# Kernel optimization log

Hardware: AMD Instinct MI355X
Metric: run time of the kernel (lower is better)

Reference implementation:

```python
import jax, jax.numpy as jnp
import numpy as np

B, T, IN, H, K = 128, 4096, 2, 64, 2  # batch, seq_len, input feat, lstm hidden, num tags


def setup_inputs() -> dict:
    key = jax.random.key(0)
    ks = jax.random.split(key, 16)
    s = 1.0 / np.sqrt(H)
    u = lambda k, shape, a: jax.random.uniform(k, shape, jnp.float32, -a, a)
    p = {}
    p['x'] = jax.random.normal(ks[0], (B, T, IN), jnp.float32)
    # layer 0 (input IN), layer 1 (input 2H); leading dim 2 = [forward, backward] direction
    p['w_ih0'] = u(ks[1], (2, 4 * H, IN), s)
    p['w_hh0'] = u(ks[2], (2, 4 * H, H), s)
    p['b_ih0'] = u(ks[3], (2, 4 * H), s)
    p['b_hh0'] = u(ks[4], (2, 4 * H), s)
    p['w_ih1'] = u(ks[5], (2, 4 * H, 2 * H), s)
    p['w_hh1'] = u(ks[6], (2, 4 * H, H), s)
    p['b_ih1'] = u(ks[7], (2, 4 * H), s)
    p['b_hh1'] = u(ks[8], (2, 4 * H), s)
    p['fc_w'] = u(ks[9], (K, 2 * H), 1.0 / np.sqrt(2 * H))
    p['fc_b'] = u(ks[10], (K,), 1.0 / np.sqrt(2 * H))
    # CRF params (torchcrf init: U(-0.1, 0.1))
    p['trans'] = u(ks[11], (K, K), 0.1)
    p['start'] = u(ks[12], (K,), 0.1)
    p['end'] = u(ks[13], (K,), 0.1)
    return p


def _lstm_dir(xg, w_hh, b_hh):
    # xg: [T, B, 4H] precomputed input projections; PyTorch gate order i, f, g, o
    b, h = xg.shape[1], w_hh.shape[1]

    def step(carry, g_x):
        hs, cs = carry
        g = g_x + hs @ w_hh.T + b_hh
        i, f, gg, o = jnp.split(g, 4, axis=-1)
        cs = jax.nn.sigmoid(f) * cs + jax.nn.sigmoid(i) * jnp.tanh(gg)
        hs = jax.nn.sigmoid(o) * jnp.tanh(cs)
        return (hs, cs), hs

    init = (jnp.zeros((b, h), xg.dtype), jnp.zeros((b, h), xg.dtype))
    _, out = jax.lax.scan(step, init, xg)
    return out  # [T, B, H]


def _bilstm_layer(xt, w_ih, w_hh, b_ih, b_hh):
    # xt: [T, B, F] time-major input
    xg_f = jnp.einsum('tbi,gi->tbg', xt, w_ih[0]) + b_ih[0]
    xg_b = jnp.einsum('tbi,gi->tbg', xt[::-1], w_ih[1]) + b_ih[1]
    hf = _lstm_dir(xg_f, w_hh[0], b_hh[0])
    hb = _lstm_dir(xg_b, w_hh[1], b_hh[1])[::-1]
    return jnp.concatenate([hf, hb], axis=-1)  # [T, B, 2H]


def _viterbi(logits, trans, start, end):
    # logits: [B, T, K] -> best path [B, T]
    e = jnp.swapaxes(logits, 0, 1)  # [T, B, K]
    score0 = start[None, :] + e[0]

    def fwd(score, e_t):
        cand = score[:, :, None] + trans[None, :, :]  # [B, Kprev, Knext]
        bp = jnp.argmax(cand, axis=1)
        return jnp.max(cand, axis=1) + e_t, bp

    score, bps = jax.lax.scan(fwd, score0, e[1:])  # bps: [T-1, B, K]
    last = jnp.argmax(score + end[None, :], axis=-1)  # [B]

    def back(tag, bp):
        prev = jnp.take_along_axis(bp, tag[:, None], axis=1)[:, 0]
        return prev, prev

    _, path = jax.lax.scan(back, last, bps, reverse=True)  # [T-1, B]
    return jnp.swapaxes(jnp.concatenate([path, last[None, :]], axis=0), 0, 1)


def reference(x, w_ih0, w_hh0, b_ih0, b_hh0, w_ih1, w_hh1, b_ih1, b_hh1,
              fc_w, fc_b, trans, start, end):
    xt = jnp.swapaxes(x, 0, 1)  # [T, B, IN]
    h0 = _bilstm_layer(xt, w_ih0, w_hh0, b_ih0, b_hh0)
    h1 = _bilstm_layer(h0, w_ih1, w_hh1, b_ih1, b_hh1)  # [T, B, 2H]
    logits = jnp.swapaxes(jnp.einsum('tbh,kh->tbk', h1, fc_w) + fc_b, 0, 1)  # [B, T, K]
    return _viterbi(logits, trans, start, end).astype(jnp.int32)
```

## Files before the change

kernel.cpp:

```cpp
#include <hip/hip_runtime.h>

#define TT 4096
#define BATCH 128
#define HID 64
#define CK 32
#define NCH (TT / CK)
#define NSLOT (NCH + 1)
#define TG 64

__device__ __forceinline__ float sigm(float x) { return 1.f / (1.f + expf(-x)); }
__device__ __forceinline__ float tanh_f(float x) { float e = expf(2.f * x); return 1.f - 2.f / (e + 1.f); }

__global__ __launch_bounds__(512, 2) void lstm_ckpt(
    const float* __restrict__ x,
    const float* __restrict__ w_ih,
    const float* __restrict__ w_hh,
    const float* __restrict__ b_ih, const float* __restrict__ b_hh,
    float* __restrict__ ckpt)
{
    const int blk = blockIdx.x;
    const int dir = blk & 1;
    const int b   = blk >> 1;
    const int tid = threadIdx.x;
    const int row = tid >> 1, half = tid & 1;

    __shared__ __align__(16) float xs[TT * 2];
    __shared__ __align__(16) float h_lds[HID];
    __shared__ __align__(16) float g_lds[256];

    {
        const float4* src = (const float4*)(x + (size_t)b * TT * 2);
        float4* dst = (float4*)xs;
        for (int rr = tid; rr < 2048; rr += 512) dst[rr] = src[rr];
    }
    const int grow = dir * 256 + row;
    float wv[32];
    {
        const float4* wr = (const float4*)(w_hh + (size_t)grow * 64) + half * 8;
        #pragma unroll
        for (int k = 0; k < 8; ++k) {
            float4 v = wr[k];
            wv[4*k] = v.x; wv[4*k+1] = v.y; wv[4*k+2] = v.z; wv[4*k+3] = v.w;
        }
    }
    const float wx0 = half ? 0.f : w_ih[grow * 2 + 0];
    const float wx1 = half ? 0.f : w_ih[grow * 2 + 1];
    const float bias = half ? 0.f : (b_ih[grow] + b_hh[grow]);
    const int gtype = row >> 6;
    float c = 0.f, hreg = 0.f;
    if (tid < HID) h_lds[tid] = 0.f;
    __syncthreads();

    for (int t = 0; t < TT; ++t) {
        const int tt = dir ? (TT - 1 - t) : t;
        if (tid < HID) {
            const int bnum = dir ? (tt + 1) : tt;
            if ((bnum & (CK - 1)) == 0) {
                float* cp = ckpt + (((size_t)(dir * BATCH + b) * NSLOT + (bnum >> 5)) << 7);
                cp[tid] = hreg; cp[HID + tid] = c;
            }
        }
        const float4* h4 = (const float4*)h_lds + half * 8;
        float a0 = 0.f, a1 = 0.f, a2 = 0.f, a3 = 0.f;
        #pragma unroll
        for (int k = 0; k < 8; ++k) {
            float4 hv = h4[k];
            a0 = fmaf(wv[4*k],   hv.x, a0);
            a1 = fmaf(wv[4*k+1], hv.y, a1);
            a2 = fmaf(wv[4*k+2], hv.z, a2);
            a3 = fmaf(wv[4*k+3], hv.w, a3);
        }
        float tot = (a0 + a1) + (a2 + a3);
        tot += __shfl_xor(tot, 1);
        if (half == 0) {
            const float acc = tot + bias + wx0 * xs[tt * 2] + wx1 * xs[tt * 2 + 1];
            g_lds[row] = (gtype == 2) ? tanh_f(acc) : sigm(acc);
        }
        __syncthreads();
        if (tid < HID) {
            const float iv = g_lds[tid], fv = g_lds[64 + tid], gg = g_lds[128 + tid], ov = g_lds[192 + tid];
            c = fv * c + iv * gg;
            hreg = ov * tanh_f(c);
            h_lds[tid] = hreg;
        }
        __syncthreads();
    }
}

__global__ __launch_bounds__(256, 4) void l0_xg(
    const float* __restrict__ x,
    const float* __restrict__ w_ih0, const float* __restrict__ w_hh0,
    const float* __restrict__ b_ih0, const float* __restrict__ b_hh0,
    const float* __restrict__ w_ih1, const float* __restrict__ b_ih1,
    const float* __restrict__ ckpt,
    float* __restrict__ xg,
    int slab_t0)
{
    const int ntg = gridDim.x / BATCH;
    const int b  = blockIdx.x / ntg;
    const int tg = blockIdx.x % ntg;
    const int T0 = slab_t0 + tg * TG;
    const int tid = threadIdx.x;
    const int e = tid & 63;
    const int cupd = tid >> 6;

    __shared__ __align__(16) float h0b[TG][128];
    __shared__ __align__(16) float hs[2][64];
    __shared__ __align__(16) float gg[2][256];
    __shared__ __align__(16) float xb[TG][2];

    if (tid < 32)
        ((float4*)xb)[tid] = ((const float4*)(x + ((size_t)b * TT + T0) * 2))[tid];

    float wl0[64];
    for (int dir = 0; dir < 2; ++dir) {
        const int rowg = dir * 256 + tid;
        {
            const float4* wa = (const float4*)(w_hh0 + (size_t)rowg * 64);
            #pragma unroll
            for (int k = 0; k < 16; ++k) {
                float4 v = wa[k];
                wl0[4*k] = v.x; wl0[4*k+1] = v.y; wl0[4*k+2] = v.z; wl0[4*k+3] = v.w;
            }
        }
        const float wx0 = w_ih0[rowg * 2 + 0], wx1 = w_ih0[rowg * 2 + 1];
        const float biasr = b_ih0[rowg] + b_hh0[rowg];
        float c_st = 0.f;
        if (tid < 128) {
            const int C = T0 / CK + cupd;
            const int slot = dir ? (C + 1) : C;
            const float* cp = ckpt + (((size_t)(dir * BATCH + b) * NSLOT + slot) << 7);
            hs[cupd][e] = cp[e];
            c_st = cp[HID + e];
        }
        __syncthreads();
        for (int s = 0; s < CK; ++s) {
            float res[2];
            #pragma unroll
            for (int c = 0; c < 2; ++c) {
                const float4* h4 = (const float4*)hs[c];
                float a0 = 0.f, a1 = 0.f, a2 = 0.f, a3 = 0.f;
                #pragma unroll
                for (int k = 0; k < 16; ++k) {
                    float4 hv = h4[k];
                    a0 = fmaf(wl0[4*k],   hv.x, a0);
                    a1 = fmaf(wl0[4*k+1], hv.y, a1);
                    a2 = fmaf(wl0[4*k+2], hv.z, a2);
                    a3 = fmaf(wl0[4*k+3], hv.w, a3);
                }
                const int tl = c * CK + (dir ? (CK - 1 - s) : s);
                res[c] = biasr + ((a0 + a1) + (a2 + a3)) + wx0 * xb[tl][0] + wx1 * xb[tl][1];
            }
            #pragma unroll
            for (int c = 0; c < 2; ++c)
                gg[c][tid] = ((tid >> 6) == 2) ? tanh_f(res[c]) : sigm(res[c]);
            __syncthreads();
            if (tid < 128) {
                const float iv = gg[cupd][e], fv = gg[cupd][64 + e], g2 = gg[cupd][128 + e], ov = gg[cupd][192 + e];
                c_st = fv * c_st + iv * g2;
                const float hv = ov * tanh_f(c_st);
                const int tl = cupd * CK + (dir ? (CK - 1 - s) : s);
                hs[cupd][e] = hv;
                h0b[tl][dir * 64 + e] = hv;
            }
            __syncthreads();
        }
    }
    for (int l1dir = 0; l1dir < 2; ++l1dir) {
        const float4* wrow = (const float4*)(w_ih1 + (size_t)(l1dir * 256 + tid) * 128);
        const float br = b_ih1[l1dir * 256 + tid];
        for (int halfT = 0; halfT < 2; ++halfT) {
            float acc[32];
            #pragma unroll
            for (int s2 = 0; s2 < 32; ++s2) acc[s2] = br;
            for (int kq = 0; kq < 32; ++kq) {
                float4 wc = wrow[kq];
                #pragma unroll
                for (int s2 = 0; s2 < 32; ++s2) {
                    float4 hv = *(const float4*)&h0b[halfT * 32 + s2][kq * 4];
                    acc[s2] = fmaf(wc.w, hv.w, fmaf(wc.z, hv.z, fmaf(wc.y, hv.y, fmaf(wc.x, hv.x, acc[s2]))));
                }
            }
            for (int s2 = 0; s2 < 32; ++s2) {
                const int tl = halfT * 32 + s2;
                xg[(((size_t)(tg * TG + tl) * BATCH + b) * 2 + l1dir) * 256 + tid] = acc[s2];
            }
        }
    }
}

__global__ __launch_bounds__(256, 2) void lstm_l1(
    const float* __restrict__ w_hh1, const float* __restrict__ b_hh1,
    const float* __restrict__ fc_w,
    const float* __restrict__ xg,
    float* __restrict__ hc1,
    float* __restrict__ plog,
    int slab_t0, int slabT)
{
    const int blk = blockIdx.x;
    const int l1dir = blk & 1;
    const int b = blk >> 1;
    const int tid = threadIdx.x;
    const int lane = tid & 63;

    __shared__ __align__(16) float h1b[2][HID];
    __shared__ __align__(16) float g1[256];
    __shared__ __align__(16) float xq[4][256];

    float wl1[64];
    {
        const int grow = l1dir * 256 + tid;
        const float4* wh = (const float4*)(w_hh1 + (size_t)grow * 64);
        #pragma unroll
        for (int k = 0; k < 16; ++k) {
            float4 v = wh[k];
            wl1[4*k] = v.x; wl1[4*k+1] = v.y; wl1[4*k+2] = v.z; wl1[4*k+3] = v.w;
        }
    }
    const float bias1 = b_hh1[l1dir * 256 + tid];
    float fw0 = 0.f, fw1 = 0.f;
    if (tid >= 64 && tid < 128) {
        fw0 = fc_w[l1dir * 64 + lane];
        fw1 = fc_w[128 + l1dir * 64 + lane];
    }
    float c1 = 0.f;
    float* hcme = hc1 + (size_t)blk * 128;
    if (tid < 64) {
        if (slab_t0 == 0) { h1b[0][tid] = 0.f; c1 = 0.f; }
        else { h1b[0][tid] = hcme[tid]; c1 = hcme[64 + tid]; }
    }
    const float* xgb = xg + ((size_t)b * 2 + l1dir) * 256;
    const size_t tstride = (size_t)BATCH * 2 * 256;
    if (tid < 128) {
        const int stp = tid >> 6;
        if (stp < slabT)
            ((float4*)xq[stp])[lane] = ((const float4*)(xgb + (size_t)stp * tstride))[lane];
    }
    float4 pend = make_float4(0.f, 0.f, 0.f, 0.f);
    if (tid >= 64 && tid < 192) {
        const int tgt = (tid < 128) ? 2 : 3;
        if (tgt < slabT) pend = ((const float4*)(xgb + (size_t)tgt * tstride))[lane];
    }
    __syncthreads();

    for (int tt = 0; tt < slabT; ++tt) {
        const int u = slab_t0 + tt;
        const int cur = tt & 1;
        {
            const float4* h4 = (const float4*)h1b[cur];
            float a0 = 0.f, a1 = 0.f, a2 = 0.f, a3 = 0.f;
            #pragma unroll
            for (int k = 0; k < 16; ++k) {
                float4 hv = h4[k];
                a0 = fmaf(wl1[4*k],   hv.x, a0);
                a1 = fmaf(wl1[4*k+1], hv.y, a1);
                a2 = fmaf(wl1[4*k+2], hv.z, a2);
                a3 = fmaf(wl1[4*k+3], hv.w, a3);
            }
            const float acc = bias1 + xq[tt & 3][tid] + ((a0 + a1) + (a2 + a3));
            g1[tid] = ((tid >> 6) == 2) ? tanh_f(acc) : sigm(acc);
        }
        __syncthreads();
        if (tid < 64) {
            const float iv = g1[tid], fv = g1[64 + tid], gg = g1[128 + tid], ov = g1[192 + tid];
            c1 = fv * c1 + iv * gg;
            h1b[cur ^ 1][tid] = ov * tanh_f(c1);
        } else if (tid < 192) {
            if (tid < 128 && u > 0) {
                const float hv = h1b[cur][lane];
                float p0 = hv * fw0, p1 = hv * fw1;
                #pragma unroll
                for (int d_ = 32; d_ > 0; d_ >>= 1) { p0 += __shfl_xor(p0, d_); p1 += __shfl_xor(p1, d_); }
                if (lane == 0) {
                    const int tp = l1dir ? (TT - u) : (u - 1);
                    *(float2*)(plog + (((size_t)l1dir * BATCH + b) * TT + tp) * 2) = make_float2(p0, p1);
                }
            }
            const int par = (tid < 128) ? 0 : 1;
            if ((tt & 1) == par) {
                if (tt + 2 < slabT) ((float4*)xq[(tt + 2) & 3])[lane] = pend;
                if (tt + 4 < slabT) pend = ((const float4*)(xgb + (size_t)(tt + 4) * tstride))[lane];
            }
        }
        __syncthreads();
    }
    if (tid < 64) { hcme[tid] = h1b[slabT & 1][tid]; hcme[64 + tid] = c1; }
    if (slab_t0 + slabT == TT && tid >= 64 && tid < 128) {
        const float hv = h1b[slabT & 1][lane];
        float p0 = hv * fw0, p1 = hv * fw1;
        #pragma unroll
        for (int d_ = 32; d_ > 0; d_ >>= 1) { p0 += __shfl_xor(p0, d_); p1 += __shfl_xor(p1, d_); }
        if (lane == 0) {
            const int tp = l1dir ? 0 : (TT - 1);
            *(float2*)(plog + (((size_t)l1dir * BATCH + b) * TT + tp) * 2) = make_float2(p0, p1);
        }
    }
}

__device__ __forceinline__ unsigned long long shfl_u64(unsigned long long v, int src) {
    unsigned int lo = (unsigned int)v, hi = (unsigned int)(v >> 32);
    lo = __shfl(lo, src); hi = __shfl(hi, src);
    return ((unsigned long long)hi << 32) | lo;
}

__global__ __launch_bounds__(64, 1) void viterbi_k(
    const float* __restrict__ plog, const float* __restrict__ fc_b,
    const float* __restrict__ trans, const float* __restrict__ startv,
    const float* __restrict__ endv, int* __restrict__ out)
{
    const int b = blockIdx.x;
    const int lane = threadIdx.x;
    __shared__ __align__(16) float2 e_lds[64][65];

    const float fb0 = fc_b[0], fb1 = fc_b[1];
    const float* pf = plog + ((size_t)(0 * BATCH + b) * TT) * 2;
    const float* pb = plog + ((size_t)(1 * BATCH + b) * TT) * 2;
    for (int r = 0; r < 32; ++r) {
        const int i4 = r * 64 + lane;
        float4 a = ((const float4*)pf)[i4];
        float4 cc = ((const float4*)pb)[i4];
        const int t0 = 2 * i4, t1 = t0 + 1;
        e_lds[t0 & 63][t0 >> 6] = make_float2(a.x + cc.x + fb0, a.y + cc.y + fb1);
        e_lds[t1 & 63][t1 >> 6] = make_float2(a.z + cc.z + fb0, a.w + cc.w + fb1);
    }
    __syncthreads();
    const float tr00 = trans[0], tr01 = trans[1], tr10 = trans[2], tr11 = trans[3];
    const float2 e0 = e_lds[0][0];
    const float s00 = startv[0] + e0.x, s01 = startv[1] + e0.y;

    const int lo = lane * 64;
    const int hi = (lane == 63) ? (TT - 1) : (lo + 64);
    float a00, a01, a10, a11;
    {
        const float2 ee = e_lds[(lo + 1) & 63][(lo + 1) >> 6];
        a00 = tr00 + ee.x; a01 = tr01 + ee.y; a10 = tr10 + ee.x; a11 = tr11 + ee.y;
    }
    for (int t = lo + 2; t <= hi; ++t) {
        const float2 ee = e_lds[t & 63][t >> 6];
        const float n00 = fmaxf(a00 + tr00, a01 + tr10) + ee.x;
        const float n01 = fmaxf(a00 + tr01, a01 + tr11) + ee.y;
        const float n10 = fmaxf(a10 + tr00, a11 + tr10) + ee.x;
        const float n11 = fmaxf(a10 + tr01, a11 + tr11) + ee.y;
        a00 = n00; a01 = n01; a10 = n10; a11 = n11;
    }
    #pragma unroll
    for (int d = 1; d < 64; d <<= 1) {
        const float o00 = __shfl_up(a00, d), o01 = __shfl_up(a01, d);
        const float o10 = __shfl_up(a10, d), o11 = __shfl_up(a11, d);
        if (lane >= d) {
            const float n00 = fmaxf(o00 + a00, o01 + a10);
            const float n01 = fmaxf(o00 + a01, o01 + a11);
            const float n10 = fmaxf(o10 + a00, o11 + a10);
            const float n11 = fmaxf(o10 + a01, o11 + a11);
            a00 = n00; a01 = n01; a10 = n10; a11 = n11;
        }
    }
    const float p00 = __shfl_up(a00, 1), p01 = __shfl_up(a01, 1);
    const float p10 = __shfl_up(a10, 1), p11 = __shfl_up(a11, 1);
    float s0, s1;
    if (lane == 0) { s0 = s00; s1 = s01; }
    else { s0 = fmaxf(s00 + p00, s01 + p10); s1 = fmaxf(s00 + p01, s01 + p11); }
    unsigned long long m0 = 0ull, m1 = 0ull;
    for (int t = lo + 1; t <= hi; ++t) {
        const float2 ee = e_lds[t & 63][t >> 6];
        const float c00 = s0 + tr00, c10 = s1 + tr10;
        const float c01 = s0 + tr01, c11 = s1 + tr11;
        const int bp0 = c10 > c00, bp1 = c11 > c01;
        s0 = (bp0 ? c10 : c00) + ee.x;
        s1 = (bp1 ? c11 : c01) + ee.y;
        m0 |= (unsigned long long)bp0 << (t - lo - 1);
        m1 |= (unsigned long long)bp1 << (t - lo - 1);
    }
    int last;
    {
        const int lt = (s1 + endv[1]) > (s0 + endv[0]);
        last = __shfl(lt, 63);
    }
    int f0 = 0, f1 = 1;
    for (int t = hi; t > lo; --t) {
        const int s_ = t - lo - 1;
        f0 = (int)(((f0 ? m1 : m0) >> s_) & 1ull);
        f1 = (int)(((f1 ? m1 : m0) >> s_) & 1ull);
    }
    int mm = f0 | (f1 << 1);
    #pragma unroll
    for (int d = 1; d < 64; d <<= 1) {
        const int mo = __shfl_down(mm, d);
        if (lane + d < 64) {
            const int r0 = (mm >> (mo & 1)) & 1;
            const int r1_ = (mm >> ((mo >> 1) & 1)) & 1;
            mm = r0 | (r1_ << 1);
        }
    }
    const int gn = __shfl_down(mm, 1);
    int cur = (lane == 63) ? last : ((gn >> last) & 1);
    unsigned long long tagm = 0ull;
    if (lane == 63) tagm |= (unsigned long long)last << 63;
    for (int t = hi; t > lo; --t) {
        const int s_ = t - lo - 1;
        cur = (int)(((cur ? m1 : m0) >> s_) & 1ull);
        tagm |= (unsigned long long)cur << s_;
    }
    int* ob = out + (size_t)b * TT;
    for (int r = 0; r < 64; ++r) {
        const unsigned long long mr = shfl_u64(tagm, r);
        ob[r * 64 + lane] = (int)((mr >> lane) & 1ull);
    }
}

extern "C" void kernel_launch(void* const* d_in, const int* in_sizes, int n_in,
                              void* d_out, int out_size, void* d_ws, size_t ws_size,
                              hipStream_t stream) {
    const float* x      = (const float*)d_in[0];
    const float* w_ih0  = (const float*)d_in[1];
    const float* w_hh0  = (const float*)d_in[2];
    const float* b_ih0  = (const float*)d_in[3];
    const float* b_hh0  = (const float*)d_in[4];
    const float* w_ih1  = (const float*)d_in[5];
    const float* w_hh1  = (const float*)d_in[6];
    const float* b_ih1  = (const float*)d_in[7];
    const float* b_hh1  = (const float*)d_in[8];
    const float* fc_w   = (const float*)d_in[9];
    const float* fc_b   = (const float*)d_in[10];
    const float* trans  = (const float*)d_in[11];
    const float* startv = (const float*)d_in[12];
    const float* endv   = (const float*)d_in[13];

    char* ws = (char*)d_ws;
    const size_t ckpt_bytes = (size_t)2 * BATCH * NSLOT * 128 * 4;
    const size_t plog_bytes = (size_t)2 * BATCH * TT * 2 * 4;
    const size_t hc1_bytes  = (size_t)256 * 128 * 4;
    float* ckpt = (float*)ws;
    float* plog = (float*)(ws + ckpt_bytes);
    float* hc1  = (float*)(ws + ckpt_bytes + plog_bytes);
    float* xg   = (float*)(ws + ckpt_bytes + plog_bytes + hc1_bytes);

    const size_t perT = (size_t)BATCH * 2 * 256 * 4;
    const size_t fixed = ckpt_bytes + plog_bytes + hc1_bytes;
    size_t avail = (ws_size > fixed) ? (ws_size - fixed) : 0;
    int slabT = (int)(avail / perT);
    slabT = (slabT / TG) * TG;
    if (slabT > TT) slabT = TT;
    if (slabT < TG) slabT = TG;

    lstm_ckpt<<<256, 512, 0, stream>>>(x, w_ih0, w_hh0, b_ih0, b_hh0, ckpt);
    for (int t0 = 0; t0 < TT; t0 += slabT) {
        const int curT = (TT - t0 < slabT) ? (TT - t0) : slabT;
        l0_xg<<<BATCH * (curT / TG), 256, 0, stream>>>(x, w_ih0, w_hh0, b_ih0, b_hh0,
                                                       w_ih1, b_ih1, ckpt, xg, t0);
        lstm_l1<<<256, 256, 0, stream>>>(w_hh1, b_hh1, fc_w, xg, hc1, plog, t0, curT);
    }
    viterbi_k<<<128, 64, 0, stream>>>(plog, fc_b, trans, startv, endv, (int*)d_out);
}
```

Before: 8.860 ms.

## Exchange LSTM gates via warp shuffles to drop one barrier per timestep

Both recurrent LSTM kernels now place each hidden unit's four gate rows in the same group of 8 adjacent lanes. The gates are combined with xor shuffles instead of going through shared memory, which removes one __syncthreads per timestep and double-buffers h. Layer 1 grows from 256 to 576 threads: 512 threads split each gate dot product in half, and a separate 64-thread wave handles the FC projection and the xg prefetch. In exchange, every thread now runs the cell-update transcendentals redundantly, and the larger block may limit occupancy.

```diff
diff --git a/kernel.cpp b/kernel.cpp
--- a/kernel.cpp
+++ b/kernel.cpp
@@ -22,67 +22,71 @@
     const int dir = blk & 1;
     const int b   = blk >> 1;
     const int tid = threadIdx.x;
-    const int row = tid >> 1, half = tid & 1;
+    const int e    = tid >> 3;
+    const int q    = (tid >> 1) & 3;
+    const int half = tid & 1;
+    const int sub  = tid & 7;
 
     __shared__ __align__(16) float xs[TT * 2];
-    __shared__ __align__(16) float h_lds[HID];
-    __shared__ __align__(16) float g_lds[256];
+    __shared__ __align__(16) float hb[2][HID];
 
     {
         const float4* src = (const float4*)(x + (size_t)b * TT * 2);
         float4* dst = (float4*)xs;
         for (int rr = tid; rr < 2048; rr += 512) dst[rr] = src[rr];
     }
-    const int grow = dir * 256 + row;
-    float wv[32];
+    const int row = dir * 256 + q * 64 + e;
+    float wl[32];
     {
-        const float4* wr = (const float4*)(w_hh + (size_t)grow * 64) + half * 8;
+        const float4* wr = (const float4*)(w_hh + (size_t)row * 64) + half * 8;
         #pragma unroll
         for (int k = 0; k < 8; ++k) {
             float4 v = wr[k];
-            wv[4*k] = v.x; wv[4*k+1] = v.y; wv[4*k+2] = v.z; wv[4*k+3] = v.w;
-        }
-    }
-    const float wx0 = half ? 0.f : w_ih[grow * 2 + 0];
-    const float wx1 = half ? 0.f : w_ih[grow * 2 + 1];
-    const float bias = half ? 0.f : (b_ih[grow] + b_hh[grow]);
-    const int gtype = row >> 6;
-    float c = 0.f, hreg = 0.f;
-    if (tid < HID) h_lds[tid] = 0.f;
+            wl[4*k] = v.x; wl[4*k+1] = v.y; wl[4*k+2] = v.z; wl[4*k+3] = v.w;
+        }
+    }
+    const float wx0 = w_ih[row * 2 + 0], wx1 = w_ih[row * 2 + 1];
+    const float bias = b_ih[row] + b_hh[row];
+    float c = 0.f, h = 0.f;
+    if (tid < HID) hb[0][tid] = 0.f;
     __syncthreads();
 
     for (int t = 0; t < TT; ++t) {
         const int tt = dir ? (TT - 1 - t) : t;
-        if (tid < HID) {
+        const int cur = t & 1;
+        {
             const int bnum = dir ? (tt + 1) : tt;
-            if ((bnum & (CK - 1)) == 0) {
+            if ((bnum & (CK - 1)) == 0 && sub == 0) {
                 float* cp = ckpt + (((size_t)(dir * BATCH + b) * NSLOT + (bnum >> 5)) << 7);
-                cp[tid] = hreg; cp[HID + tid] = c;
-            }
-        }
-        const float4* h4 = (const float4*)h_lds + half * 8;
+                cp[e] = h; cp[HID + e] = c;
+            }
+        }
+        const float4* h4 = (const float4*)hb[cur] + half * 8;
         float a0 = 0.f, a1 = 0.f, a2 = 0.f, a3 = 0.f;
         #pragma unroll
         for (int k = 0; k < 8; ++k) {
             float4 hv = h4[k];
-            a0 = fmaf(wv[4*k],   hv.x, a0);
-            a1 = fmaf(wv[4*k+1], hv.y, a1);
-            a2 = fmaf(wv[4*k+2], hv.z, a2);
-            a3 = fmaf(wv[4*k+3], hv.w, a3);
+            a0 = fmaf(wl[4*k],   hv.x, a0);
+            a1 = fmaf(wl[4*k+1], hv.y, a1);
+            a2 = fmaf(wl[4*k+2], hv.z, a2);
+            a3 = fmaf(wl[4*k+3], hv.w, a3);
         }
         float tot = (a0 + a1) + (a2 + a3);
         tot += __shfl_xor(tot, 1);
-        if (half == 0) {
-            const float acc = tot + bias + wx0 * xs[tt * 2] + wx1 * xs[tt * 2 + 1];
-            g_lds[row] = (gtype == 2) ? tanh_f(acc) : sigm(acc);
-        }
-        __syncthreads();
-        if (tid < HID) {
-            const float iv = g_lds[tid], fv = g_lds[64 + tid], gg = g_lds[128 + tid], ov = g_lds[192 + tid];
-            c = fv * c + iv * gg;
-            hreg = ov * tanh_f(c);
-            h_lds[tid] = hreg;
-        }
+        const float2 xv = *(const float2*)&xs[tt * 2];
+        tot += bias + wx0 * xv.x + wx1 * xv.y;
+        const float av = (q == 2) ? tanh_f(tot) : sigm(tot);
+        const float bv = __shfl_xor(av, 2);
+        const float cv = __shfl_xor(av, 4);
+        const float dv = __shfl_xor(bv, 4);
+        float iv, fv, gv, ov;
+        if      (q == 0) { iv = av; fv = bv; gv = cv; ov = dv; }
+        else if (q == 1) { iv = bv; fv = av; gv = dv; ov = cv; }
+        else if (q == 2) { iv = cv; fv = dv; gv = av; ov = bv; }
+        else             { iv = dv; fv = cv; gv = bv; ov = av; }
+        c = fv * c + iv * gv;
+        h = ov * tanh_f(c);
+        if (sub == 0) hb[cur ^ 1][e] = h;
         __syncthreads();
     }
 }
@@ -189,7 +193,7 @@
     }
 }
 
-__global__ __launch_bounds__(256, 2) void lstm_l1(
+__global__ __launch_bounds__(576, 1) void lstm_l1(
     const float* __restrict__ w_hh1, const float* __restrict__ b_hh1,
     const float* __restrict__ fc_w,
     const float* __restrict__ xg,
@@ -201,96 +205,104 @@
     const int l1dir = blk & 1;
     const int b = blk >> 1;
     const int tid = threadIdx.x;
-    const int lane = tid & 63;
+    const bool isGate = tid < 512;
+    const int e    = tid >> 3;
+    const int q    = (tid >> 1) & 3;
+    const int half = tid & 1;
+    const int sub  = tid & 7;
+    const int lane9 = tid - 512;
 
     __shared__ __align__(16) float h1b[2][HID];
-    __shared__ __align__(16) float g1[256];
     __shared__ __align__(16) float xq[4][256];
 
-    float wl1[64];
-    {
-        const int grow = l1dir * 256 + tid;
-        const float4* wh = (const float4*)(w_hh1 + (size_t)grow * 64);
-        #pragma unroll
-        for (int k = 0; k < 16; ++k) {
-            float4 v = wh[k];
-            wl1[4*k] = v.x; wl1[4*k+1] = v.y; wl1[4*k+2] = v.z; wl1[4*k+3] = v.w;
-        }
-    }
-    const float bias1 = b_hh1[l1dir * 256 + tid];
-    float fw0 = 0.f, fw1 = 0.f;
-    if (tid >= 64 && tid < 128) {
-        fw0 = fc_w[l1dir * 64 + lane];
-        fw1 = fc_w[128 + l1dir * 64 + lane];
-    }
-    float c1 = 0.f;
-    float* hcme = hc1 + (size_t)blk * 128;
-    if (tid < 64) {
-        if (slab_t0 == 0) { h1b[0][tid] = 0.f; c1 = 0.f; }
-        else { h1b[0][tid] = hcme[tid]; c1 = hcme[64 + tid]; }
-    }
+    float wl[32];
+    float bias1 = 0.f, fw0 = 0.f, fw1 = 0.f;
+    float c1 = 0.f, h = 0.f;
+    float4 pend0 = make_float4(0.f,0.f,0.f,0.f), pend1 = make_float4(0.f,0.f,0.f,0.f);
     const float* xgb = xg + ((size_t)b * 2 + l1dir) * 256;
     const size_t tstride = (size_t)BATCH * 2 * 256;
-    if (tid < 128) {
-        const int stp = tid >> 6;
-        if (stp < slabT)
-            ((float4*)xq[stp])[lane] = ((const float4*)(xgb + (size_t)stp * tstride))[lane];
-    }
-    float4 pend = make_float4(0.f, 0.f, 0.f, 0.f);
-    if (tid >= 64 && tid < 192) {
-        const int tgt = (tid < 128) ? 2 : 3;
-        if (tgt < slabT) pend = ((const float4*)(xgb + (size_t)tgt * tstride))[lane];
+    float* hcme = hc1 + (size_t)blk * 128;
+
+    if (isGate) {
+        const int grow = l1dir * 256 + q * 64 + e;
+        const float4* wr = (const float4*)(w_hh1 + (size_t)grow * 64) + half * 8;
+        #pragma unroll
+        for (int k = 0; k < 8; ++k) {
+            float4 v = wr[k];
+            wl[4*k] = v.x; wl[4*k+1] = v.y; wl[4*k+2] = v.z; wl[4*k+3] = v.w;
+        }
+        bias1 = b_hh1[grow];
+        if (slab_t0 == 0) { h = 0.f; c1 = 0.f; }
+        else { h = hcme[e]; c1 = hcme[64 + e]; }
+        if (sub == 0) h1b[0][e] = h;
+    } else {
+        fw0 = fc_w[l1dir * 64 + lane9];
+        fw1 = fc_w[128 + l1dir * 64 + lane9];
+        #pragma unroll
+        for (int s = 0; s < 3; ++s)
+            if (s < slabT)
+                ((float4*)xq[s])[lane9] = ((const float4*)(xgb + (size_t)s * tstride))[lane9];
+        if (3 < slabT) pend0 = ((const float4*)(xgb + (size_t)3 * tstride))[lane9];
+        if (4 < slabT) pend1 = ((const float4*)(xgb + (size_t)4 * tstride))[lane9];
     }
     __syncthreads();
 
     for (int tt = 0; tt < slabT; ++tt) {
-        const int u = slab_t0 + tt;
         const int cur = tt & 1;
-        {
-            const float4* h4 = (const float4*)h1b[cur];
+        if (isGate) {
+            const float4* h4 = (const float4*)h1b[cur] + half * 8;
             float a0 = 0.f, a1 = 0.f, a2 = 0.f, a3 = 0.f;
             #pragma unroll
-            for (int k = 0; k < 16; ++k) {
+            for (int k = 0; k < 8; ++k) {
                 float4 hv = h4[k];
-                a0 = fmaf(wl1[4*k],   hv.x, a0);
-                a1 = fmaf(wl1[4*k+1], hv.y, a1);
-                a2 = fmaf(wl1[4*k+2], hv.z, a2);
-                a3 = fmaf(wl1[4*k+3], hv.w, a3);
-            }
-            const float acc = bias1 + xq[tt & 3][tid] + ((a0 + a1) + (a2 + a3));
-            g1[tid] = ((tid >> 6) == 2) ? tanh_f(acc) : sigm(acc);
-        }
-        __syncthreads();
-        if (tid < 64) {
-            const float iv = g1[tid], fv = g1[64 + tid], gg = g1[128 + tid], ov = g1[192 + tid];
-            c1 = fv * c1 + iv * gg;
-            h1b[cur ^ 1][tid] = ov * tanh_f(c1);
-        } else if (tid < 192) {
-            if (tid < 128 && u > 0) {
-                const float hv = h1b[cur][lane];
+                a0 = fmaf(wl[4*k],   hv.x, a0);
+                a1 = fmaf(wl[4*k+1], hv.y, a1);
+                a2 = fmaf(wl[4*k+2], hv.z, a2);
+                a3 = fmaf(wl[4*k+3], hv.w, a3);
+            }
+            float tot = (a0 + a1) + (a2 + a3);
+            tot += __shfl_xor(tot, 1);
+            tot += bias1 + xq[tt & 3][q * 64 + e];
+            const float av = (q == 2) ? tanh_f(tot) : sigm(tot);
+            const float bv = __shfl_xor(av, 2);
+            const float cv = __shfl_xor(av, 4);
+            const float dv = __shfl_xor(bv, 4);
+            float iv, fv, gv, ov;
+            if      (q == 0) { iv = av; fv = bv; gv = cv; ov = dv; }
+            else if (q == 1) { iv = bv; fv = av; gv = dv; ov = cv; }
+            else if (q == 2) { iv = cv; fv = dv; gv = av; ov = bv; }
+            else             { iv = dv; fv = cv; gv = bv; ov = av; }
+            c1 = fv * c1 + iv * gv;
+            h = ov * tanh_f(c1);
+            if (sub == 0) h1b[cur ^ 1][e] = h;
+        } else {
+            const int u = slab_t0 + tt;
+            if (u > 0) {
+                const float hv = h1b[cur][lane9];
                 float p0 = hv * fw0, p1 = hv * fw1;
                 #pragma unroll
                 for (int d_ = 32; d_ > 0; d_ >>= 1) { p0 += __shfl_xor(p0, d_); p1 += __shfl_xor(p1, d_); }
-                if (lane == 0) {
+                if (lane9 == 0) {
                     const int tp = l1dir ? (TT - u) : (u - 1);
                     *(float2*)(plog + (((size_t)l1dir * BATCH + b) * TT + tp) * 2) = make_float2(p0, p1);
                 }
             }
-            const int par = (tid < 128) ? 0 : 1;
-            if ((tt & 1) == par) {
-                if (tt + 2 < slabT) ((float4*)xq[(tt + 2) & 3])[lane] = pend;
-                if (tt + 4 < slabT) pend = ((const float4*)(xgb + (size_t)(tt + 4) * tstride))[lane];
+            if (tt + 3 < slabT)
+                ((float4*)xq[(tt + 3) & 3])[lane9] = (tt & 1) ? pend1 : pend0;
+            if (tt + 5 < slabT) {
+                float4 nl = ((const float4*)(xgb + (size_t)(tt + 5) * tstride))[lane9];
+                if (tt & 1) pend1 = nl; else pend0 = nl;
             }
         }
         __syncthreads();
     }
-    if (tid < 64) { hcme[tid] = h1b[slabT & 1][tid]; hcme[64 + tid] = c1; }
-    if (slab_t0 + slabT == TT && tid >= 64 && tid < 128) {
-        const float hv = h1b[slabT & 1][lane];
+    if (isGate && sub == 0) { hcme[e] = h; hcme[64 + e] = c1; }
+    if (!isGate && slab_t0 + slabT == TT) {
+        const float hv = h1b[slabT & 1][lane9];
         float p0 = hv * fw0, p1 = hv * fw1;
         #pragma unroll
         for (int d_ = 32; d_ > 0; d_ >>= 1) { p0 += __shfl_xor(p0, d_); p1 += __shfl_xor(p1, d_); }
-        if (lane == 0) {
+        if (lane9 == 0) {
             const int tp = l1dir ? 0 : (TT - 1);
             *(float2*)(plog + (((size_t)l1dir * BATCH + b) * TT + tp) * 2) = make_float2(p0, p1);
         }
@@ -448,7 +460,7 @@
         const int curT = (TT - t0 < slabT) ? (TT - t0) : slabT;
         l0_xg<<<BATCH * (curT / TG), 256, 0, stream>>>(x, w_ih0, w_hh0, b_ih0, b_hh0,
                                                        w_ih1, b_ih1, ckpt, xg, t0);
-        lstm_l1<<<256, 256, 0, stream>>>(w_hh1, b_hh1, fc_w, xg, hc1, plog, t0, curT);
+        lstm_l1<<<256, 576, 0, stream>>>(w_hh1, b_hh1, fc_w, xg, hc1, plog, t0, curT);
     }
     viterbi_k<<<128, 64, 0, stream>>>(plog, fc_b, trans, startv, endv, (int*)d_out);
 }
```

Result: slower. 10.26 ms (+15.8%).
